# Kernel optimization log

Measured on AMD Instinct MI355X. Metric: run time of the kernel, lower is better.

Reference implementation:

```python
import jax, jax.numpy as jnp
import numpy as np

D_MODEL = 1024
NUM_HEADS = 16
D_K = D_MODEL // NUM_HEADS


def setup_inputs() -> dict:
    key = jax.random.key(0)
    ks = jax.random.split(key, 11)
    B, S = 4, 2048
    s = 1.0 / np.sqrt(D_MODEL)
    inp = {
        "q": jax.random.normal(ks[0], (B, S, D_MODEL), jnp.float32),
        "k": jax.random.normal(ks[1], (B, S, D_MODEL), jnp.float32),
        "v": jax.random.normal(ks[2], (B, S, D_MODEL), jnp.float32),
        "Wq": jax.random.normal(ks[3], (D_MODEL, D_MODEL), jnp.float32) * s,
        "bq": jnp.zeros((D_MODEL,), jnp.float32),
        "Wk": jax.random.normal(ks[4], (D_MODEL, D_MODEL), jnp.float32) * s,
        "bk": jnp.zeros((D_MODEL,), jnp.float32),
        "Wv": jax.random.normal(ks[5], (D_MODEL, D_MODEL), jnp.float32) * s,
        "bv": jnp.zeros((D_MODEL,), jnp.float32),
        "Wo": jax.random.normal(ks[6], (D_MODEL, D_MODEL), jnp.float32) * s,
        "bo": jnp.zeros((D_MODEL,), jnp.float32),
    }
    return inp


def reference(q, k, v, Wq, bq, Wk, bk, Wv, bv, Wo, bo):
    B, S, _ = q.shape
    # QKV projections, then split heads: [B,S,D] -> [B,H,S,d_k]
    def split_heads(x):
        return x.reshape(B, -1, NUM_HEADS, D_K).transpose(0, 2, 1, 3)
    Q = split_heads(q @ Wq + bq)
    K = split_heads(k @ Wk + bk)
    V = split_heads(v @ Wv + bv)
    # scaled dot-product attention (mask=None, dropout p=0 -> identity)
    scores = jnp.einsum("bhqd,bhkd->bhqk", Q, K) / jnp.sqrt(jnp.float32(D_K))
    attn = jax.nn.softmax(scores, axis=-1)
    out = jnp.einsum("bhqk,bhkd->bhqd", attn, V)
    out = out.transpose(0, 2, 1, 3).reshape(B, -1, D_MODEL)
    return out @ Wo + bo
```

## Files before the change

kernel.cpp:

```cpp
#include <hip/hip_runtime.h>

#define MB (1ull << 20)

typedef __attribute__((ext_vector_type(8))) short bf16x8;
typedef __attribute__((ext_vector_type(4))) float f32x4;

#if defined(__has_builtin)
#if __has_builtin(__builtin_amdgcn_global_load_lds)
#define HAS_GLL 1
#endif
#endif
#ifndef HAS_GLL
#define HAS_GLL 0
#endif

__device__ __forceinline__ unsigned short f2bf(float f) {
  unsigned u = __float_as_uint(f);
  u += 0x7fffu + ((u >> 16) & 1u);
  return (unsigned short)(u >> 16);
}

#if HAS_GLL
__device__ __forceinline__ void gl16(const unsigned short* g, unsigned short* l) {
  __builtin_amdgcn_global_load_lds((const __attribute__((address_space(1))) void*)g,
                                   (__attribute__((address_space(3))) void*)l, 16, 0, 0);
}
#endif

__global__ __launch_bounds__(256) void cvt_f32_bf16(const float* __restrict__ x,
                                                    unsigned short* __restrict__ y, int n) {
  int i = (blockIdx.x * 256 + threadIdx.x) * 4;
  if (i >= n) return;
  float4 v = *(const float4*)(x + i);
  uint2 p;
  p.x = (unsigned)f2bf(v.x) | ((unsigned)f2bf(v.y) << 16);
  p.y = (unsigned)f2bf(v.z) | ((unsigned)f2bf(v.w) << 16);
  *(uint2*)(y + i) = p;
}

__global__ __launch_bounds__(256) void transpose_cvt(const float* __restrict__ W,
                                                     unsigned short* __restrict__ WT) {
  __shared__ float tile[32][33];
  int bx = blockIdx.x * 32;
  int by = blockIdx.y * 32;
  int tx = threadIdx.x, ty = threadIdx.y;
#pragma unroll
  for (int i = 0; i < 32; i += 8)
    tile[ty + i][tx] = W[(by + ty + i) * 1024 + bx + tx];
  __syncthreads();
#pragma unroll
  for (int i = 0; i < 32; i += 8)
    WT[(bx + ty + i) * 1024 + by + tx] = f2bf(tile[tx][ty + i]);
}

template <int MODE>
__global__ __launch_bounds__(256) void gemm_bt(const unsigned short* __restrict__ A,
                                               const unsigned short* __restrict__ Bt,
                                               const float* __restrict__ bias,
                                               void* __restrict__ Cout, int M, int N, int K,
                                               float scale) {
  __shared__ __align__(16) unsigned short As[128 * 32];
  __shared__ __align__(16) unsigned short Bs[128 * 32];
  const int tid = threadIdx.x;
  const int wave = tid >> 6, lane = tid & 63;
  const int quad = lane >> 4, r = lane & 15;
  const int m0 = blockIdx.y * 128, n0 = blockIdx.x * 128;
  const int wm = (wave >> 1) * 64, wn = (wave & 1) * 64;

  const int srow = tid >> 2;
  const int scol = (tid & 3) * 8;
  const unsigned short* Ag0 = A + (size_t)(m0 + srow) * K + scol;
  const unsigned short* Ag1 = A + (size_t)(m0 + 64 + srow) * K + scol;
  const unsigned short* Bg0 = Bt + (size_t)(n0 + srow) * K + scol;
  const unsigned short* Bg1 = Bt + (size_t)(n0 + 64 + srow) * K + scol;

  f32x4 acc[4][4] = {};

#if HAS_GLL
  for (int k0 = 0; k0 < K; k0 += 32) {
    __syncthreads();
    gl16(Ag0 + k0, As + tid * 8);
    gl16(Ag1 + k0, As + 2048 + tid * 8);
    gl16(Bg0 + k0, Bs + tid * 8);
    gl16(Bg1 + k0, Bs + 2048 + tid * 8);
    __syncthreads();
    bf16x8 af[4], bfr[4];
#pragma unroll
    for (int i = 0; i < 4; ++i)
      af[i] = *(const bf16x8*)(As + (wm + i * 16 + r) * 32 + quad * 8);
#pragma unroll
    for (int j = 0; j < 4; ++j)
      bfr[j] = *(const bf16x8*)(Bs + (wn + j * 16 + r) * 32 + quad * 8);
#pragma unroll
    for (int i = 0; i < 4; ++i)
#pragma unroll
      for (int j = 0; j < 4; ++j)
        acc[i][j] = __builtin_amdgcn_mfma_f32_16x16x32_bf16(af[i], bfr[j], acc[i][j], 0, 0, 0);
  }
#else
  uint4* AsW0 = (uint4*)(As + tid * 8);
  uint4* AsW1 = (uint4*)(As + 2048 + tid * 8);
  uint4* BsW0 = (uint4*)(Bs + tid * 8);
  uint4* BsW1 = (uint4*)(Bs + 2048 + tid * 8);
  for (int k0 = 0; k0 < K; k0 += 32) {
    uint4 a0 = *(const uint4*)(Ag0 + k0);
    uint4 a1 = *(const uint4*)(Ag1 + k0);
    uint4 b0 = *(const uint4*)(Bg0 + k0);
    uint4 b1 = *(const uint4*)(Bg1 + k0);
    __syncthreads();
    *AsW0 = a0;
    *AsW1 = a1;
    *BsW0 = b0;
    *BsW1 = b1;
    __syncthreads();
    bf16x8 af[4], bfr[4];
#pragma unroll
    for (int i = 0; i < 4; ++i)
      af[i] = *(const bf16x8*)(As + (wm + i * 16 + r) * 32 + quad * 8);
#pragma unroll
    for (int j = 0; j < 4; ++j)
      bfr[j] = *(const bf16x8*)(Bs + (wn + j * 16 + r) * 32 + quad * 8);
#pragma unroll
    for (int i = 0; i < 4; ++i)
#pragma unroll
      for (int j = 0; j < 4; ++j)
        acc[i][j] = __builtin_amdgcn_mfma_f32_16x16x32_bf16(af[i], bfr[j], acc[i][j], 0, 0, 0);
  }
#endif

#pragma unroll
  for (int i = 0; i < 4; ++i) {
#pragma unroll
    for (int j = 0; j < 4; ++j) {
      const int col = n0 + wn + j * 16 + r;
      const float bv = bias[col];
      if (MODE == 3) {
        const int b = m0 >> 11;
        const int rloc = (m0 & 2047) + wm + i * 16 + quad * 4;
        float v0 = (acc[i][j][0] + bv) * scale;
        float v1 = (acc[i][j][1] + bv) * scale;
        float v2 = (acc[i][j][2] + bv) * scale;
        float v3 = (acc[i][j][3] + bv) * scale;
        uint2 u;
        u.x = ((unsigned)f2bf(v1) << 16) | f2bf(v0);
        u.y = ((unsigned)f2bf(v3) << 16) | f2bf(v2);
        *(uint2*)((unsigned short*)Cout + ((size_t)(b * N + col)) * 2048 + rloc) = u;
      } else {
#pragma unroll
        for (int t = 0; t < 4; ++t) {
          const int row = m0 + wm + i * 16 + quad * 4 + t;
          float v = (acc[i][j][t] + bv) * scale;
          if (MODE == 1)
            ((unsigned short*)Cout)[(size_t)row * N + col] = f2bf(v);
          else
            ((float*)Cout)[(size_t)row * N + col] = v;
        }
      }
    }
  }
}

__global__ __launch_bounds__(256) void flash_mfma(const unsigned short* __restrict__ Qb,
                                                  const unsigned short* __restrict__ Kb,
                                                  const unsigned short* __restrict__ Vt,
                                                  unsigned short* __restrict__ Ob) {
  __shared__ __align__(16) unsigned short Ksh[64 * 72];
  __shared__ __align__(16) unsigned short Vts[64 * 72];
  __shared__ __align__(16) unsigned short Ps[4 * 64 * 72];
  const int tid = threadIdx.x;
  const int wave = tid >> 6, lane = tid & 63;
  const int quad = lane >> 4, r = lane & 15;
  const int b = blockIdx.y >> 4, h = blockIdx.y & 15;
  const int qbase = b * 2048 + blockIdx.x * 256 + wave * 64;

  bf16x8 qf[4][2];
#pragma unroll
  for (int jq = 0; jq < 4; ++jq)
#pragma unroll
    for (int ks = 0; ks < 2; ++ks)
      qf[jq][ks] = *(const bf16x8*)(Qb + (size_t)(qbase + jq * 16 + r) * 1024 + h * 64 +
                                    ks * 32 + quad * 8);

  f32x4 oacc[4][4] = {};
  float lp[4] = {0.f, 0.f, 0.f, 0.f};

  const int srow = tid >> 2, sc = (tid & 3) * 16;
  const unsigned short* Kg = Kb + (size_t)(b * 2048 + srow) * 1024 + h * 64 + sc;
  const unsigned short* Vg = Vt + (size_t)(b * 1024 + h * 64 + srow) * 2048 + sc;
  unsigned short* PsW = Ps + wave * (64 * 72);

  for (int kt0 = 0; kt0 < 32; ++kt0) {
    uint4 ka = *(const uint4*)Kg;
    uint4 kb2 = *(const uint4*)(Kg + 8);
    uint4 va = *(const uint4*)Vg;
    uint4 vb2 = *(const uint4*)(Vg + 8);
    Kg += 64 * 1024;
    Vg += 64;
    __syncthreads();
    *(uint4*)(Ksh + srow * 72 + sc) = ka;
    *(uint4*)(Ksh + srow * 72 + sc + 8) = kb2;
    *(uint4*)(Vts + srow * 72 + sc) = va;
    *(uint4*)(Vts + srow * 72 + sc + 8) = vb2;
    __syncthreads();

    bf16x8 kf[4][2];
#pragma unroll
    for (int kt = 0; kt < 4; ++kt)
#pragma unroll
      for (int ks = 0; ks < 2; ++ks)
        kf[kt][ks] = *(const bf16x8*)(Ksh + (kt * 16 + r) * 72 + ks * 32 + quad * 8);

#pragma unroll
    for (int jq = 0; jq < 4; ++jq) {
      f32x4 st[4] = {};
#pragma unroll
      for (int ks = 0; ks < 2; ++ks)
#pragma unroll
        for (int kt = 0; kt < 4; ++kt)
          st[kt] = __builtin_amdgcn_mfma_f32_16x16x32_bf16(kf[kt][ks], qf[jq][ks], st[kt], 0, 0, 0);
#pragma unroll
      for (int kt = 0; kt < 4; ++kt) {
        float p0 = __builtin_amdgcn_exp2f(st[kt][0]);
        float p1 = __builtin_amdgcn_exp2f(st[kt][1]);
        float p2 = __builtin_amdgcn_exp2f(st[kt][2]);
        float p3 = __builtin_amdgcn_exp2f(st[kt][3]);
        lp[jq] += (p0 + p1) + (p2 + p3);
        uint2 u;
        u.x = __builtin_amdgcn_perm(__float_as_uint(p1) + 0x8000u,
                                    __float_as_uint(p0) + 0x8000u, 0x07060302u);
        u.y = __builtin_amdgcn_perm(__float_as_uint(p3) + 0x8000u,
                                    __float_as_uint(p2) + 0x8000u, 0x07060302u);
        *(uint2*)(PsW + (jq * 16 + r) * 72 + kt * 16 + quad * 4) = u;
      }
    }

    bf16x8 vf[4][2];
#pragma unroll
    for (int dt = 0; dt < 4; ++dt)
#pragma unroll
      for (int ks = 0; ks < 2; ++ks)
        vf[dt][ks] = *(const bf16x8*)(Vts + (dt * 16 + r) * 72 + ks * 32 + quad * 8);
#pragma unroll
    for (int jq = 0; jq < 4; ++jq)
#pragma unroll
      for (int ks = 0; ks < 2; ++ks) {
        bf16x8 pf = *(const bf16x8*)(PsW + (jq * 16 + r) * 72 + ks * 32 + quad * 8);
#pragma unroll
        for (int dt = 0; dt < 4; ++dt)
          oacc[jq][dt] = __builtin_amdgcn_mfma_f32_16x16x32_bf16(vf[dt][ks], pf, oacc[jq][dt], 0, 0, 0);
      }
  }

#pragma unroll
  for (int jq = 0; jq < 4; ++jq) {
    float l = lp[jq];
    l += __shfl_xor(l, 16);
    l += __shfl_xor(l, 32);
    float inv = 1.0f / l;
#pragma unroll
    for (int dt = 0; dt < 4; ++dt) {
      float v0 = oacc[jq][dt][0] * inv, v1 = oacc[jq][dt][1] * inv;
      float v2 = oacc[jq][dt][2] * inv, v3 = oacc[jq][dt][3] * inv;
      uint2 u;
      u.x = ((unsigned)f2bf(v1) << 16) | f2bf(v0);
      u.y = ((unsigned)f2bf(v3) << 16) | f2bf(v2);
      *(uint2*)(Ob + (size_t)(qbase + jq * 16 + r) * 1024 + h * 64 + dt * 16 + quad * 4) = u;
    }
  }
}

extern "C" void kernel_launch(void* const* d_in, const int* in_sizes, int n_in, void* d_out,
                              int out_size, void* d_ws, size_t ws_size, hipStream_t stream) {
  const float* q = (const float*)d_in[0];
  const float* k = (const float*)d_in[1];
  const float* v = (const float*)d_in[2];
  const float* Wq = (const float*)d_in[3];
  const float* bq = (const float*)d_in[4];
  const float* Wk = (const float*)d_in[5];
  const float* bk = (const float*)d_in[6];
  const float* Wv = (const float*)d_in[7];
  const float* bv = (const float*)d_in[8];
  const float* Wo = (const float*)d_in[9];
  const float* bo = (const float*)d_in[10];

  unsigned char* ws = (unsigned char*)d_ws;
  unsigned short* qb = (unsigned short*)(ws + 0 * MB);
  unsigned short* kb = (unsigned short*)(ws + 16 * MB);
  unsigned short* vb = (unsigned short*)(ws + 32 * MB);
  unsigned short* WqT = (unsigned short*)(ws + 48 * MB);
  unsigned short* WkT = (unsigned short*)(ws + 50 * MB);
  unsigned short* WvT = (unsigned short*)(ws + 52 * MB);
  unsigned short* WoT = (unsigned short*)(ws + 54 * MB);
  unsigned short* Qb = (unsigned short*)(ws + 56 * MB);
  unsigned short* Kbf = (unsigned short*)(ws + 72 * MB);
  unsigned short* Vtr = (unsigned short*)(ws + 88 * MB);
  unsigned short* AOb = (unsigned short*)(ws + 104 * MB);

  const int M = 8192, D = 1024;
  const float c2 = 0.18033688011112042f;

  cvt_f32_bf16<<<M * D / 1024, 256, 0, stream>>>(q, qb, M * D);
  cvt_f32_bf16<<<M * D / 1024, 256, 0, stream>>>(k, kb, M * D);
  cvt_f32_bf16<<<M * D / 1024, 256, 0, stream>>>(v, vb, M * D);

  dim3 tb(32, 8), tg(32, 32);
  transpose_cvt<<<tg, tb, 0, stream>>>(Wq, WqT);
  transpose_cvt<<<tg, tb, 0, stream>>>(Wk, WkT);
  transpose_cvt<<<tg, tb, 0, stream>>>(Wv, WvT);
  transpose_cvt<<<tg, tb, 0, stream>>>(Wo, WoT);

  dim3 gg(D / 128, M / 128);
  gemm_bt<1><<<gg, 256, 0, stream>>>(qb, WqT, bq, Qb, M, D, D, c2);
  gemm_bt<1><<<gg, 256, 0, stream>>>(kb, WkT, bk, Kbf, M, D, D, 1.0f);
  gemm_bt<3><<<gg, 256, 0, stream>>>(vb, WvT, bv, Vtr, M, D, D, 1.0f);

  flash_mfma<<<dim3(8, 64), 256, 0, stream>>>(Qb, Kbf, Vtr, AOb);

  gemm_bt<0><<<gg, 256, 0, stream>>>(AOb, WoT, bo, d_out, M, D, D, 1.0f);
}
```

Before: 393.6 us.

## Batch launches, swizzle LDS with BK=64 in GEMMs, shrink flash P buffer

Measured after the change: 393.9 us. About the same (+0.1%).

```diff
diff --git a/kernel.cpp b/kernel.cpp
--- a/kernel.cpp
+++ b/kernel.cpp
@@ -27,8 +27,15 @@
 }
 #endif
 
-__global__ __launch_bounds__(256) void cvt_f32_bf16(const float* __restrict__ x,
-                                                    unsigned short* __restrict__ y, int n) {
+__global__ __launch_bounds__(256) void cvt3(const float* __restrict__ x0,
+                                            const float* __restrict__ x1,
+                                            const float* __restrict__ x2,
+                                            unsigned short* __restrict__ y0,
+                                            unsigned short* __restrict__ y1,
+                                            unsigned short* __restrict__ y2, int n) {
+  const int z = blockIdx.y;
+  const float* x = (z == 0) ? x0 : (z == 1) ? x1 : x2;
+  unsigned short* y = (z == 0) ? y0 : (z == 1) ? y1 : y2;
   int i = (blockIdx.x * 256 + threadIdx.x) * 4;
   if (i >= n) return;
   float4 v = *(const float4*)(x + i);
@@ -38,12 +45,21 @@
   *(uint2*)(y + i) = p;
 }
 
-__global__ __launch_bounds__(256) void transpose_cvt(const float* __restrict__ W,
-                                                     unsigned short* __restrict__ WT) {
+__global__ __launch_bounds__(256) void transpose4(const float* __restrict__ W0,
+                                                  const float* __restrict__ W1,
+                                                  const float* __restrict__ W2,
+                                                  const float* __restrict__ W3,
+                                                  unsigned short* __restrict__ T0,
+                                                  unsigned short* __restrict__ T1,
+                                                  unsigned short* __restrict__ T2,
+                                                  unsigned short* __restrict__ T3) {
+  const int z = blockIdx.z;
+  const float* W = (z == 0) ? W0 : (z == 1) ? W1 : (z == 2) ? W2 : W3;
+  unsigned short* WT = (z == 0) ? T0 : (z == 1) ? T1 : (z == 2) ? T2 : T3;
   __shared__ float tile[32][33];
   int bx = blockIdx.x * 32;
   int by = blockIdx.y * 32;
-  int tx = threadIdx.x, ty = threadIdx.y;
+  int tx = threadIdx.x & 31, ty = threadIdx.x >> 5;
 #pragma unroll
   for (int i = 0; i < 32; i += 8)
     tile[ty + i][tx] = W[(by + ty + i) * 1024 + bx + tx];
@@ -53,120 +69,146 @@
     WT[(bx + ty + i) * 1024 + by + tx] = f2bf(tile[tx][ty + i]);
 }
 
-template <int MODE>
-__global__ __launch_bounds__(256) void gemm_bt(const unsigned short* __restrict__ A,
-                                               const unsigned short* __restrict__ Bt,
-                                               const float* __restrict__ bias,
-                                               void* __restrict__ Cout, int M, int N, int K,
-                                               float scale) {
-  __shared__ __align__(16) unsigned short As[128 * 32];
-  __shared__ __align__(16) unsigned short Bs[128 * 32];
+__device__ __forceinline__ void gemm_core(const unsigned short* __restrict__ A,
+                                          const unsigned short* __restrict__ Bt, int K, int m0,
+                                          int n0, unsigned short* As, unsigned short* Bs,
+                                          f32x4 (&acc)[4][4]) {
   const int tid = threadIdx.x;
   const int wave = tid >> 6, lane = tid & 63;
   const int quad = lane >> 4, r = lane & 15;
+  const int wm = (wave >> 1) * 64, wn = (wave & 1) * 64;
+
+  const int srow8 = tid >> 3;
+  const int clog8 = ((tid & 7) ^ (srow8 & 7)) * 8;
+  const unsigned short* Ag = A + (size_t)(m0 + srow8) * K + clog8;
+  const unsigned short* Bg = Bt + (size_t)(n0 + srow8) * K + clog8;
+
+  const int cA = ((0 ^ quad) ^ (r & 7)) * 8;
+  const int cB = ((4 ^ quad) ^ (r & 7)) * 8;
+
+  for (int k0 = 0; k0 < K; k0 += 64) {
+    __syncthreads();
+#if HAS_GLL
+#pragma unroll
+    for (int s = 0; s < 4; ++s) {
+      gl16(Ag + (size_t)(s * 32) * K + k0, As + s * 2048 + tid * 8);
+      gl16(Bg + (size_t)(s * 32) * K + k0, Bs + s * 2048 + tid * 8);
+    }
+#else
+#pragma unroll
+    for (int s = 0; s < 4; ++s) {
+      uint4 a = *(const uint4*)(Ag + (size_t)(s * 32) * K + k0);
+      uint4 b = *(const uint4*)(Bg + (size_t)(s * 32) * K + k0);
+      *(uint4*)(As + s * 2048 + tid * 8) = a;
+      *(uint4*)(Bs + s * 2048 + tid * 8) = b;
+    }
+#endif
+    __syncthreads();
+#pragma unroll
+    for (int ks = 0; ks < 2; ++ks) {
+      const int co = ks ? cB : cA;
+      bf16x8 af[4], bfr[4];
+#pragma unroll
+      for (int i = 0; i < 4; ++i) af[i] = *(const bf16x8*)(As + (wm + i * 16 + r) * 64 + co);
+#pragma unroll
+      for (int j = 0; j < 4; ++j) bfr[j] = *(const bf16x8*)(Bs + (wn + j * 16 + r) * 64 + co);
+#pragma unroll
+      for (int i = 0; i < 4; ++i)
+#pragma unroll
+        for (int j = 0; j < 4; ++j)
+          acc[i][j] = __builtin_amdgcn_mfma_f32_16x16x32_bf16(af[i], bfr[j], acc[i][j], 0, 0, 0);
+    }
+  }
+}
+
+__global__ __launch_bounds__(256) void gemm_qkv(
+    const unsigned short* __restrict__ A0, const unsigned short* __restrict__ A1,
+    const unsigned short* __restrict__ A2, const unsigned short* __restrict__ B0,
+    const unsigned short* __restrict__ B1, const unsigned short* __restrict__ B2,
+    const float* __restrict__ b0, const float* __restrict__ b1, const float* __restrict__ b2,
+    unsigned short* __restrict__ O0, unsigned short* __restrict__ O1,
+    unsigned short* __restrict__ O2, int M, int N, int K, float scaleQ) {
+  __shared__ __align__(16) unsigned short As[128 * 64];
+  __shared__ __align__(16) unsigned short Bs[128 * 64];
+  const int z = blockIdx.z;
+  const unsigned short* A = (z == 0) ? A0 : (z == 1) ? A1 : A2;
+  const unsigned short* Bt = (z == 0) ? B0 : (z == 1) ? B1 : B2;
+  const float* bias = (z == 0) ? b0 : (z == 1) ? b1 : b2;
+  const float scale = (z == 0) ? scaleQ : 1.0f;
   const int m0 = blockIdx.y * 128, n0 = blockIdx.x * 128;
+
+  f32x4 acc[4][4] = {};
+  gemm_core(A, Bt, K, m0, n0, As, Bs, acc);
+
+  const int lane = threadIdx.x & 63, wave = threadIdx.x >> 6;
+  const int quad = lane >> 4, r = lane & 15;
   const int wm = (wave >> 1) * 64, wn = (wave & 1) * 64;
 
-  const int srow = tid >> 2;
-  const int scol = (tid & 3) * 8;
-  const unsigned short* Ag0 = A + (size_t)(m0 + srow) * K + scol;
-  const unsigned short* Ag1 = A + (size_t)(m0 + 64 + srow) * K + scol;
-  const unsigned short* Bg0 = Bt + (size_t)(n0 + srow) * K + scol;
-  const unsigned short* Bg1 = Bt + (size_t)(n0 + 64 + srow) * K + scol;
-
+  if (z < 2) {
+    unsigned short* Cout = (z == 0) ? O0 : O1;
+#pragma unroll
+    for (int i = 0; i < 4; ++i)
+#pragma unroll
+      for (int j = 0; j < 4; ++j) {
+        const int col = n0 + wn + j * 16 + r;
+        const float bv = bias[col];
+#pragma unroll
+        for (int t = 0; t < 4; ++t) {
+          const int row = m0 + wm + i * 16 + quad * 4 + t;
+          Cout[(size_t)row * N + col] = f2bf((acc[i][j][t] + bv) * scale);
+        }
+      }
+  } else {
+    const int b = m0 >> 11;
+#pragma unroll
+    for (int i = 0; i < 4; ++i)
+#pragma unroll
+      for (int j = 0; j < 4; ++j) {
+        const int col = n0 + wn + j * 16 + r;
+        const float bv = bias[col];
+        const int rloc = (m0 & 2047) + wm + i * 16 + quad * 4;
+        uint2 u;
+        u.x = ((unsigned)f2bf(acc[i][j][1] + bv) << 16) | f2bf(acc[i][j][0] + bv);
+        u.y = ((unsigned)f2bf(acc[i][j][3] + bv) << 16) | f2bf(acc[i][j][2] + bv);
+        *(uint2*)(O2 + ((size_t)(b * N + col)) * 2048 + rloc) = u;
+      }
+  }
+}
+
+__global__ __launch_bounds__(256) void gemm_o(const unsigned short* __restrict__ A,
+                                              const unsigned short* __restrict__ Bt,
+                                              const float* __restrict__ bias,
+                                              float* __restrict__ Cout, int M, int N, int K) {
+  __shared__ __align__(16) unsigned short As[128 * 64];
+  __shared__ __align__(16) unsigned short Bs[128 * 64];
+  const int m0 = blockIdx.y * 128, n0 = blockIdx.x * 128;
   f32x4 acc[4][4] = {};
-
-#if HAS_GLL
-  for (int k0 = 0; k0 < K; k0 += 32) {
-    __syncthreads();
-    gl16(Ag0 + k0, As + tid * 8);
-    gl16(Ag1 + k0, As + 2048 + tid * 8);
-    gl16(Bg0 + k0, Bs + tid * 8);
-    gl16(Bg1 + k0, Bs + 2048 + tid * 8);
-    __syncthreads();
-    bf16x8 af[4], bfr[4];
-#pragma unroll
-    for (int i = 0; i < 4; ++i)
-      af[i] = *(const bf16x8*)(As + (wm + i * 16 + r) * 32 + quad * 8);
-#pragma unroll
-    for (int j = 0; j < 4; ++j)
-      bfr[j] = *(const bf16x8*)(Bs + (wn + j * 16 + r) * 32 + quad * 8);
-#pragma unroll
-    for (int i = 0; i < 4; ++i)
-#pragma unroll
-      for (int j = 0; j < 4; ++j)
-        acc[i][j] = __builtin_amdgcn_mfma_f32_16x16x32_bf16(af[i], bfr[j], acc[i][j], 0, 0, 0);
-  }
-#else
-  uint4* AsW0 = (uint4*)(As + tid * 8);
-  uint4* AsW1 = (uint4*)(As + 2048 + tid * 8);
-  uint4* BsW0 = (uint4*)(Bs + tid * 8);
-  uint4* BsW1 = (uint4*)(Bs + 2048 + tid * 8);
-  for (int k0 = 0; k0 < K; k0 += 32) {
-    uint4 a0 = *(const uint4*)(Ag0 + k0);
-    uint4 a1 = *(const uint4*)(Ag1 + k0);
-    uint4 b0 = *(const uint4*)(Bg0 + k0);
-    uint4 b1 = *(const uint4*)(Bg1 + k0);
-    __syncthreads();
-    *AsW0 = a0;
-    *AsW1 = a1;
-    *BsW0 = b0;
-    *BsW1 = b1;
-    __syncthreads();
-    bf16x8 af[4], bfr[4];
-#pragma unroll
-    for (int i = 0; i < 4; ++i)
-      af[i] = *(const bf16x8*)(As + (wm + i * 16 + r) * 32 + quad * 8);
-#pragma unroll
-    for (int j = 0; j < 4; ++j)
-      bfr[j] = *(const bf16x8*)(Bs + (wn + j * 16 + r) * 32 + quad * 8);
-#pragma unroll
-    for (int i = 0; i < 4; ++i)
-#pragma unroll
-      for (int j = 0; j < 4; ++j)
-        acc[i][j] = __builtin_amdgcn_mfma_f32_16x16x32_bf16(af[i], bfr[j], acc[i][j], 0, 0, 0);
-  }
-#endif
-
-#pragma unroll
-  for (int i = 0; i < 4; ++i) {
+  gemm_core(A, Bt, K, m0, n0, As, Bs, acc);
+
+  const int lane = threadIdx.x & 63, wave = threadIdx.x >> 6;
+  const int quad = lane >> 4, r = lane & 15;
+  const int wm = (wave >> 1) * 64, wn = (wave & 1) * 64;
+#pragma unroll
+  for (int i = 0; i < 4; ++i)
 #pragma unroll
     for (int j = 0; j < 4; ++j) {
       const int col = n0 + wn + j * 16 + r;
       const float bv = bias[col];
-      if (MODE == 3) {
-        const int b = m0 >> 11;
-        const int rloc = (m0 & 2047) + wm + i * 16 + quad * 4;
-        float v0 = (acc[i][j][0] + bv) * scale;
-        float v1 = (acc[i][j][1] + bv) * scale;
-        float v2 = (acc[i][j][2] + bv) * scale;
-        float v3 = (acc[i][j][3] + bv) * scale;
-        uint2 u;
-        u.x = ((unsigned)f2bf(v1) << 16) | f2bf(v0);
-        u.y = ((unsigned)f2bf(v3) << 16) | f2bf(v2);
-        *(uint2*)((unsigned short*)Cout + ((size_t)(b * N + col)) * 2048 + rloc) = u;
-      } else {
-#pragma unroll
-        for (int t = 0; t < 4; ++t) {
-          const int row = m0 + wm + i * 16 + quad * 4 + t;
-          float v = (acc[i][j][t] + bv) * scale;
-          if (MODE == 1)
-            ((unsigned short*)Cout)[(size_t)row * N + col] = f2bf(v);
-          else
-            ((float*)Cout)[(size_t)row * N + col] = v;
-        }
-      }
-    }
-  }
+#pragma unroll
+      for (int t = 0; t < 4; ++t) {
+        const int row = m0 + wm + i * 16 + quad * 4 + t;
+        Cout[(size_t)row * N + col] = acc[i][j][t] + bv;
+      }
+    }
 }
 
 __global__ __launch_bounds__(256) void flash_mfma(const unsigned short* __restrict__ Qb,
                                                   const unsigned short* __restrict__ Kb,
                                                   const unsigned short* __restrict__ Vt,
                                                   unsigned short* __restrict__ Ob) {
-  __shared__ __align__(16) unsigned short Ksh[64 * 72];
-  __shared__ __align__(16) unsigned short Vts[64 * 72];
-  __shared__ __align__(16) unsigned short Ps[4 * 64 * 72];
+  __shared__ __align__(16) unsigned short Ksh[64 * 64];
+  __shared__ __align__(16) unsigned short Vts[64 * 64];
+  __shared__ __align__(16) unsigned short Ps[4 * 16 * 64];
   const int tid = threadIdx.x;
   const int wave = tid >> 6, lane = tid & 63;
   const int quad = lane >> 4, r = lane & 15;
@@ -184,10 +226,13 @@
   f32x4 oacc[4][4] = {};
   float lp[4] = {0.f, 0.f, 0.f, 0.f};
 
-  const int srow = tid >> 2, sc = (tid & 3) * 16;
-  const unsigned short* Kg = Kb + (size_t)(b * 2048 + srow) * 1024 + h * 64 + sc;
-  const unsigned short* Vg = Vt + (size_t)(b * 1024 + h * 64 + srow) * 2048 + sc;
-  unsigned short* PsW = Ps + wave * (64 * 72);
+  const int srow = tid >> 2;
+  const int c0 = (tid & 3) * 2;
+  const int c0p = c0 ^ (srow & 7);
+  const unsigned short* Kg = Kb + (size_t)(b * 2048 + srow) * 1024 + h * 64 + c0 * 8;
+  const unsigned short* Vg = Vt + (size_t)(b * 1024 + h * 64 + srow) * 2048 + c0 * 8;
+  unsigned short* PsW = Ps + wave * 1024;
+  const int rx = (r & 7);
 
   for (int kt0 = 0; kt0 < 32; ++kt0) {
     uint4 ka = *(const uint4*)Kg;
@@ -197,18 +242,20 @@
     Kg += 64 * 1024;
     Vg += 64;
     __syncthreads();
-    *(uint4*)(Ksh + srow * 72 + sc) = ka;
-    *(uint4*)(Ksh + srow * 72 + sc + 8) = kb2;
-    *(uint4*)(Vts + srow * 72 + sc) = va;
-    *(uint4*)(Vts + srow * 72 + sc + 8) = vb2;
+    *(uint4*)(Ksh + srow * 64 + c0p * 8) = ka;
+    *(uint4*)(Ksh + srow * 64 + (c0p ^ 1) * 8) = kb2;
+    *(uint4*)(Vts + srow * 64 + c0p * 8) = va;
+    *(uint4*)(Vts + srow * 64 + (c0p ^ 1) * 8) = vb2;
     __syncthreads();
 
-    bf16x8 kf[4][2];
+    bf16x8 kf[4][2], vf[4][2];
 #pragma unroll
     for (int kt = 0; kt < 4; ++kt)
 #pragma unroll
-      for (int ks = 0; ks < 2; ++ks)
-        kf[kt][ks] = *(const bf16x8*)(Ksh + (kt * 16 + r) * 72 + ks * 32 + quad * 8);
+      for (int ks = 0; ks < 2; ++ks) {
+        kf[kt][ks] = *(const bf16x8*)(Ksh + (kt * 16 + r) * 64 + (((ks * 4 + quad) ^ rx) * 8));
+        vf[kt][ks] = *(const bf16x8*)(Vts + (kt * 16 + r) * 64 + (((ks * 4 + quad) ^ rx) * 8));
+      }
 
 #pragma unroll
     for (int jq = 0; jq < 4; ++jq) {
@@ -230,25 +277,16 @@
                                     __float_as_uint(p0) + 0x8000u, 0x07060302u);
         u.y = __builtin_amdgcn_perm(__float_as_uint(p3) + 0x8000u,
                                     __float_as_uint(p2) + 0x8000u, 0x07060302u);
-        *(uint2*)(PsW + (jq * 16 + r) * 72 + kt * 16 + quad * 4) = u;
-      }
-    }
-
-    bf16x8 vf[4][2];
-#pragma unroll
-    for (int dt = 0; dt < 4; ++dt)
-#pragma unroll
-      for (int ks = 0; ks < 2; ++ks)
-        vf[dt][ks] = *(const bf16x8*)(Vts + (dt * 16 + r) * 72 + ks * 32 + quad * 8);
-#pragma unroll
-    for (int jq = 0; jq < 4; ++jq)
+        *(uint2*)(PsW + r * 64 + (((kt * 2 + (quad >> 1)) ^ rx) * 8) + (quad & 1) * 4) = u;
+      }
 #pragma unroll
       for (int ks = 0; ks < 2; ++ks) {
-        bf16x8 pf = *(const bf16x8*)(PsW + (jq * 16 + r) * 72 + ks * 32 + quad * 8);
+        bf16x8 pf = *(const bf16x8*)(PsW + r * 64 + (((ks * 4 + quad) ^ rx) * 8));
 #pragma unroll
         for (int dt = 0; dt < 4; ++dt)
           oacc[jq][dt] = __builtin_amdgcn_mfma_f32_16x16x32_bf16(vf[dt][ks], pf, oacc[jq][dt], 0, 0, 0);
       }
+    }
   }
 
 #pragma unroll
@@ -259,11 +297,9 @@
     float inv = 1.0f / l;
 #pragma unroll
     for (int dt = 0; dt < 4; ++dt) {
-      float v0 = oacc[jq][dt][0] * inv, v1 = oacc[jq][dt][1] * inv;
-      float v2 = oacc[jq][dt][2] * inv, v3 = oacc[jq][dt][3] * inv;
       uint2 u;
-      u.x = ((unsigned)f2bf(v1) << 16) | f2bf(v0);
-      u.y = ((unsigned)f2bf(v3) << 16) | f2bf(v2);
+      u.x = ((unsigned)f2bf(oacc[jq][dt][1] * inv) << 16) | f2bf(oacc[jq][dt][0] * inv);
+      u.y = ((unsigned)f2bf(oacc[jq][dt][3] * inv) << 16) | f2bf(oacc[jq][dt][2] * inv);
       *(uint2*)(Ob + (size_t)(qbase + jq * 16 + r) * 1024 + h * 64 + dt * 16 + quad * 4) = u;
     }
   }
@@ -299,22 +335,13 @@
   const int M = 8192, D = 1024;
   const float c2 = 0.18033688011112042f;
 
-  cvt_f32_bf16<<<M * D / 1024, 256, 0, stream>>>(q, qb, M * D);
-  cvt_f32_bf16<<<M * D / 1024, 256, 0, stream>>>(k, kb, M * D);
-  cvt_f32_bf16<<<M * D / 1024, 256, 0, stream>>>(v, vb, M * D);
-
-  dim3 tb(32, 8), tg(32, 32);
-  transpose_cvt<<<tg, tb, 0, stream>>>(Wq, WqT);
-  transpose_cvt<<<tg, tb, 0, stream>>>(Wk, WkT);
-  transpose_cvt<<<tg, tb, 0, stream>>>(Wv, WvT);
-  transpose_cvt<<<tg, tb, 0, stream>>>(Wo, WoT);
-
-  dim3 gg(D / 128, M / 128);
-  gemm_bt<1><<<gg, 256, 0, stream>>>(qb, WqT, bq, Qb, M, D, D, c2);
-  gemm_bt<1><<<gg, 256, 0, stream>>>(kb, WkT, bk, Kbf, M, D, D, 1.0f);
-  gemm_bt<3><<<gg, 256, 0, stream>>>(vb, WvT, bv, Vtr, M, D, D, 1.0f);
+  cvt3<<<dim3(M * D / 1024, 3), 256, 0, stream>>>(q, k, v, qb, kb, vb, M * D);
+  transpose4<<<dim3(32, 32, 4), 256, 0, stream>>>(Wq, Wk, Wv, Wo, WqT, WkT, WvT, WoT);
+
+  gemm_qkv<<<dim3(D / 128, M / 128, 3), 256, 0, stream>>>(qb, kb, vb, WqT, WkT, WvT, bq, bk, bv,
+                                                          Qb, Kbf, Vtr, M, D, D, c2);
 
   flash_mfma<<<dim3(8, 64), 256, 0, stream>>>(Qb, Kbf, Vtr, AOb);
 
-  gemm_bt<0><<<gg, 256, 0, stream>>>(AOb, WoT, bo, d_out, M, D, D, 1.0f);
-}
+  gemm_o<<<dim3(D / 128, M / 128), 256, 0, stream>>>(AOb, WoT, bo, (float*)d_out, M, D, D);
+}
```
